# Kernel optimization log

Hardware: AMD Instinct MI355X
Metric: run time of the kernel (lower is better)

## Reference

```python
import jax, jax.numpy as jnp
import numpy as np
from jax import lax

B, T, C, H, W = 2, 64, 32, 64, 64   # (batch, feat-channels t, bands c, height, width)
NH = 4                              # num_heads; head dim = C//NH
HID = int(T * 2.66)                 # GDFN hidden channels = 170
EPS_LN = 1e-5
EPS_L2 = 1e-12


def _dwconv3d(x, w, pad):
    # x: (B, Cg, D, H, W); w: (Cg, 1, kd, kh, kw) depthwise
    cg = x.shape[1]
    return lax.conv_general_dilated(
        x, w, window_strides=(1, 1, 1), padding=pad,
        dimension_numbers=('NCDHW', 'OIDHW', 'NCDHW'),
        feature_group_count=cg)


def _pw(w, x):
    # 1x1x1 conv == channel GEMM; w: (out, in)
    return jnp.einsum('oi,bidhw->bodhw', w, x)


def _ln_ch(x, g, b):
    # LayerNorm over channel dim (dim1), matching reshape/transpose dance in torch
    m = jnp.mean(x, axis=1, keepdims=True)
    v = jnp.var(x, axis=1, keepdims=True)
    xn = (x - m) * lax.rsqrt(v + EPS_LN)
    return xn * g[None, :, None, None, None] + b[None, :, None, None, None]


def _attn(x, temperature, qkv_w, qkv_dw, attn_out_w):
    b, t, c, h, w = x.shape
    qkv = _dwconv3d(_pw(qkv_w, x), qkv_dw, ((0, 0), (1, 1), (1, 1)))  # (b,3t,c,h,w)
    q, k, v = jnp.split(qkv, 3, axis=1)
    L = h * w * t
    X = (t * c * h * w) // (NH * L)  # == c // NH
    rsh = lambda a: a.reshape(b, NH, X, L)
    q, k, v = rsh(q), rsh(k), rsh(v)
    l2n = lambda a: a / jnp.maximum(jnp.linalg.norm(a, axis=-1, keepdims=True), EPS_L2)
    q, k = l2n(q), l2n(k)
    scores = jnp.einsum('bnxl,bnyl->bnxy', q, k) * temperature  # (b,NH,X,X)
    att = jax.nn.softmax(scores, axis=-1)
    o = jnp.einsum('bnxy,bnyl->bnxl', att, v).reshape(b, t, c, h, w)
    return _pw(attn_out_w, o)


def _ffn(x, pin_w, dw_w, pout_w):
    y = _dwconv3d(_pw(pin_w, x), dw_w, ((1, 1), (1, 1), (1, 1)))  # (b,2*HID,c,h,w)
    x1, x2 = jnp.split(y, 2, axis=1)
    return _pw(pout_w, jax.nn.gelu(x1, approximate=False) * x2)


def setup_inputs() -> dict:
    key = jax.random.key(0)
    ks = jax.random.split(key, 12)
    s = lambda *sh: 1.0 / np.sqrt(np.prod(sh[1:]) if len(sh) > 1 else 1.0)
    p = lambda k, *sh: jax.random.normal(k, sh, dtype=jnp.float32) * s(*sh)
    return {
        'x': jax.random.normal(ks[0], (B, T, C, H, W), dtype=jnp.float32),
        'norm1_g': jnp.ones((T,), jnp.float32),
        'norm1_b': jnp.zeros((T,), jnp.float32),
        'temperature': jnp.ones((1, NH, 1, 1), jnp.float32),
        'qkv_w': p(ks[1], 3 * T, T),
        'qkv_dw': p(ks[2], 3 * T, 1, 1, 3, 3),
        'attn_out_w': p(ks[3], T, T),
        'norm2_g': jnp.ones((T,), jnp.float32),
        'norm2_b': jnp.zeros((T,), jnp.float32),
        'pin_w': p(ks[4], 2 * HID, T),
        'dw_w': p(ks[5], 2 * HID, 1, 3, 3, 3),
        'pout_w': p(ks[6], T, HID),
        'se_w': p(ks[7], T, T),
        'se_b': jnp.zeros((T,), jnp.float32),
    }


def reference(x, norm1_g, norm1_b, temperature, qkv_w, qkv_dw, attn_out_w,
              norm2_g, norm2_b, pin_w, dw_w, pout_w, se_w, se_b):
    x = x + _attn(_ln_ch(x, norm1_g, norm1_b), temperature, qkv_w, qkv_dw, attn_out_w)
    x = x + _ffn(_ln_ch(x, norm2_g, norm2_b), pin_w, dw_w, pout_w)
    s = jnp.mean(x, axis=(2, 3, 4), keepdims=True)               # GlobalAvgPool3d
    s = jax.nn.sigmoid(_pw(se_w, s) + se_b[None, :, None, None, None])
    return s * x
```

## Files before the change

kernel.cpp:

```cpp
#include <hip/hip_runtime.h>
#include <hip/hip_bf16.h>
#include <math.h>

typedef __hip_bfloat16 bf16;

#define S_ 131072

#define OFF_QKVW 0
#define OFF_AOW  12288
#define OFF_PINW 16384
#define OFF_POUTW 38912
#define OFF_SEW  49792
#define OFF_QDW  53888
#define OFF_DWW  55616
#define OFF_N1G  64796
#define OFF_N1B  64860
#define OFF_N2G  64924
#define OFF_N2B  64988
#define OFF_SEB  65052
#define OFF_TEMP 65116
#define WB_TOTAL 65120

#define SM_SSQ 0
#define SM_SSK 64
#define SM_ATT 128
#define SM_MEAN 640
#define SM_SVEC 768
#define SM_M 896
#define SM_FLAGI 9216

#define WSOFF_SM 262144
#define WSOFF_X1 303104
#define WSOFF_R  33857536
#define WS_REQUIRED 134520832ull

#define NCHUNK 256
#define PROW 44

__device__ __forceinline__ float toF(float v) { return v; }
__device__ __forceinline__ float toF(bf16 v) { return __bfloat162float(v); }

__device__ __forceinline__ float bfbitsToF(unsigned short u) {
  union { unsigned int i; float f; } x;
  x.i = ((unsigned int)u) << 16;
  return x.f;
}

__device__ __forceinline__ unsigned short bfBits(float f) {
  bf16 h = __float2bfloat16(f);
  return *reinterpret_cast<unsigned short*>(&h);
}

__device__ __forceinline__ float ldIn(const void* p, size_t i, int isbf) {
  return isbf ? __bfloat162float(((const bf16*)p)[i]) : ((const float*)p)[i];
}
__device__ __forceinline__ void stOut(void* p, size_t i, int isbf, float v) {
  if (isbf) ((bf16*)p)[i] = __float2bfloat16(v);
  else ((float*)p)[i] = v;
}

__device__ __forceinline__ float wred(float v) {
#pragma unroll
  for (int o = 32; o > 0; o >>= 1) v += __shfl_down(v, o, 64);
  return v;
}

__device__ __forceinline__ void conv4(const bf16* __restrict__ plane,
                                      const float* __restrict__ w9,
                                      int h, int w0, bool wlo, bool whi,
                                      float& o0, float& o1, float& o2, float& o3) {
  o0 = o1 = o2 = o3 = 0.f;
#pragma unroll
  for (int rr = 0; rr < 3; ++rr) {
    int hh = h - 1 + rr;
    if ((unsigned)hh < 64u) {
      const bf16* row = plane + hh * 64 + w0;
      ushort4 m = *reinterpret_cast<const ushort4*>(row);
      float v1 = bfbitsToF(m.x), v2 = bfbitsToF(m.y);
      float v3 = bfbitsToF(m.z), v4 = bfbitsToF(m.w);
      float v0 = wlo ? toF(row[-1]) : 0.f;
      float v5 = whi ? toF(row[4]) : 0.f;
      float wa = w9[rr * 3 + 0], wbb = w9[rr * 3 + 1], wc = w9[rr * 3 + 2];
      o0 = fmaf(wa, v0, fmaf(wbb, v1, fmaf(wc, v2, o0)));
      o1 = fmaf(wa, v1, fmaf(wbb, v2, fmaf(wc, v3, o1)));
      o2 = fmaf(wa, v2, fmaf(wbb, v3, fmaf(wc, v4, o2)));
      o3 = fmaf(wa, v3, fmaf(wbb, v4, fmaf(wc, v5, o3)));
    }
  }
}

__global__ void zero_sm(float* sm, const unsigned* n1g_raw) {
  for (int i = threadIdx.x; i < 768; i += 256) sm[i] = 0.f;
  if (threadIdx.x == 0) {
    ((int*)sm)[SM_FLAGI] = ((n1g_raw[0] & 0xFFFFu) != 0u) ? 1 : 0;
  }
}

__global__ void convert_w(const void* qkvw, const void* aow, const void* pinw,
                          const void* poutw, const void* sew, const void* qdw,
                          const void* dww, const void* n1g, const void* n1b,
                          const void* n2g, const void* n2b, const void* seb,
                          const void* temp, float* wb, const int* dflag) {
  int i = blockIdx.x * 256 + threadIdx.x;
  if (i >= WB_TOTAL) return;
  int f = *dflag;
  float v;
  if (i < OFF_AOW) v = ldIn(qkvw, i, f);
  else if (i < OFF_PINW) v = ldIn(aow, i - OFF_AOW, f);
  else if (i < OFF_POUTW) { int r = i - OFF_PINW; v = (r < 21760) ? ldIn(pinw, r, f) : 0.f; }
  else if (i < OFF_SEW) v = ldIn(poutw, i - OFF_POUTW, f);
  else if (i < OFF_QDW) v = ldIn(sew, i - OFF_SEW, f);
  else if (i < OFF_DWW) v = ldIn(qdw, i - OFF_QDW, f);
  else if (i < OFF_N1G) v = ldIn(dww, i - OFF_DWW, f);
  else if (i < OFF_N1B) v = ldIn(n1g, i - OFF_N1G, f);
  else if (i < OFF_N2G) v = ldIn(n1b, i - OFF_N1B, f);
  else if (i < OFF_N2B) v = ldIn(n2g, i - OFF_N2G, f);
  else if (i < OFF_SEB) v = ldIn(n2b, i - OFF_N2B, f);
  else if (i < OFF_TEMP) v = ldIn(seb, i - OFF_SEB, f);
  else v = ldIn(temp, i - OFF_TEMP, f);
  wb[i] = v;
}

__global__ __launch_bounds__(256) void qkv_ln_gemm(const void* __restrict__ x,
                                                   const float* __restrict__ wb,
                                                   bf16* __restrict__ qraw,
                                                   const int* __restrict__ dflag) {
  __shared__ bf16 tile[64][256];
  int tid = threadIdx.x;
  int p0 = blockIdx.x << 8;
  int b = p0 >> 17, s0 = p0 & (S_ - 1);
  int isbf = *dflag;
  float xin[64];
  if (isbf) {
    const bf16* src = (const bf16*)x + (size_t)b * 64 * S_ + s0;
#pragma unroll
    for (int i = 0; i < 8; ++i) {
      int q = i * 256 + tid;
      int row = q >> 5;
      int col8 = (q & 31) * 8;
      *reinterpret_cast<uint4*>(&tile[row][col8]) =
          *reinterpret_cast<const uint4*>(src + (size_t)row * S_ + col8);
    }
    __syncthreads();
#pragma unroll
    for (int t = 0; t < 64; ++t) xin[t] = toF(tile[t][tid]);
  } else {
    const float* xf = (const float*)x + (size_t)b * 64 * S_ + s0 + tid;
#pragma unroll
    for (int t = 0; t < 64; ++t) xin[t] = xf[(size_t)t * S_];
  }
  float sum = 0.f;
#pragma unroll
  for (int t = 0; t < 64; ++t) sum += xin[t];
  float mean = sum * (1.f / 64.f);
  float ss = 0.f;
#pragma unroll
  for (int t = 0; t < 64; ++t) { float d = xin[t] - mean; ss += d * d; }
  float rstd = rsqrtf(ss * (1.f / 64.f) + 1e-5f);
#pragma unroll
  for (int t = 0; t < 64; ++t)
    xin[t] = (xin[t] - mean) * rstd * wb[OFF_N1G + t] + wb[OFF_N1B + t];
  size_t obase = (size_t)b * 192 * S_ + s0 + tid;
  for (int oc = 0; oc < 192; oc += 16) {
    float acc[16];
#pragma unroll
    for (int j = 0; j < 16; ++j) acc[j] = 0.f;
    const float* wp = wb + OFF_QKVW + oc * 64;
#pragma unroll
    for (int t = 0; t < 64; ++t) {
      float xv = xin[t];
#pragma unroll
      for (int j = 0; j < 16; ++j) acc[j] = fmaf(wp[j * 64 + t], xv, acc[j]);
    }
#pragma unroll
    for (int j = 0; j < 16; ++j)
      qraw[obase + (size_t)(oc + j) * S_] = __float2bfloat16(acc[j]);
  }
}

__global__ __launch_bounds__(256, 4) void attn_scores(const bf16* __restrict__ qraw,
                                                      const float* __restrict__ wb,
                                                      float* __restrict__ part) {
  int blk = blockIdx.x;
  int bh = blk >> 9, qh = (blk >> 8) & 1, chunk = blk & (NCHUNK - 1);
  int b = bh >> 2, nh = bh & 3;
  int pbit = chunk >> 7;
  int c = (chunk >> 2) & 31;
  int hq = chunk & 3;
  int tid = threadIdx.x;
  int wseg = tid & 15, w0 = wseg * 4;
  int h = hq * 16 + (tid >> 4);
  bool wlo = (wseg != 0), whi = (wseg != 15);

  float dq[4], dk[8], dot[32], qv[4][4];
#pragma unroll
  for (int i = 0; i < 4; ++i) dq[i] = 0.f;
#pragma unroll
  for (int i = 0; i < 8; ++i) dk[i] = 0.f;
#pragma unroll
  for (int i = 0; i < 32; ++i) dot[i] = 0.f;

  const size_t bbase = ((size_t)(b * 192)) << 17;

#pragma unroll
  for (int r = 0; r < 4; ++r) {
    int ch = 2 * (nh * 8 + qh * 4 + r) + pbit;
    const bf16* pl = qraw + bbase + (((size_t)ch) << 17) + (c << 12);
    float o0, o1, o2, o3;
    conv4(pl, wb + OFF_QDW + ch * 9, h, w0, wlo, whi, o0, o1, o2, o3);
    qv[r][0] = o0; qv[r][1] = o1; qv[r][2] = o2; qv[r][3] = o3;
    dq[r] = fmaf(o0, o0, fmaf(o1, o1, fmaf(o2, o2, fmaf(o3, o3, dq[r]))));
  }
#pragma unroll
  for (int r = 0; r < 8; ++r) {
    int ch = 64 + 2 * (nh * 8 + r) + pbit;
    const bf16* pl = qraw + bbase + (((size_t)ch) << 17) + (c << 12);
    float k0, k1, k2, k3;
    conv4(pl, wb + OFF_QDW + ch * 9, h, w0, wlo, whi, k0, k1, k2, k3);
    dk[r] = fmaf(k0, k0, fmaf(k1, k1, fmaf(k2, k2, fmaf(k3, k3, dk[r]))));
#pragma unroll
    for (int i = 0; i < 4; ++i)
      dot[i * 8 + r] = fmaf(qv[i][0], k0, fmaf(qv[i][1], k1,
                       fmaf(qv[i][2], k2, fmaf(qv[i][3], k3, dot[i * 8 + r]))));
  }

  __shared__ float red[4][PROW];
  int lane = threadIdx.x & 63, wid = threadIdx.x >> 6;
#pragma unroll
  for (int i = 0; i < 4; ++i) {
    float v = wred(dq[i]);
    if (lane == 0) red[wid][i] = v;
  }
#pragma unroll
  for (int i = 0; i < 8; ++i) {
    float v = wred(dk[i]);
    if (lane == 0) red[wid][4 + i] = v;
  }
#pragma unroll
  for (int ij = 0; ij < 32; ++ij) {
    float v = wred(dot[ij]);
    if (lane == 0) red[wid][12 + ij] = v;
  }
  __syncthreads();
  if (threadIdx.x < PROW)
    part[blk * PROW + threadIdx.x] = red[0][threadIdx.x] + red[1][threadIdx.x] +
                                     red[2][threadIdx.x] + red[3][threadIdx.x];
}

__global__ void attn_reduce(const float* __restrict__ part, float* __restrict__ sm) {
  int o = blockIdx.x;
  int bh = o / 80, v = o - bh * 80;
  int qi, off;
  if (v < 8) {
    qi = v >> 2; off = v & 3;
  } else if (v < 16) {
    qi = 0; off = 4 + (v - 8);
  } else {
    int idx = v - 16;
    int i = idx >> 3, j = idx & 7;
    qi = i >> 2; off = 12 + (i & 3) * 8 + j;
  }
  __shared__ float s[256];
  s[threadIdx.x] = part[(((size_t)bh * 2 + qi) * NCHUNK + threadIdx.x) * PROW + off];
  __syncthreads();
#pragma unroll
  for (int st = 128; st > 0; st >>= 1) {
    if (threadIdx.x < st) s[threadIdx.x] += s[threadIdx.x + st];
    __syncthreads();
  }
  if (threadIdx.x == 0) {
    float r = s[0];
    if (v < 8) sm[SM_SSQ + bh * 8 + v] = r;
    else if (v < 16) sm[SM_SSK + bh * 8 + (v - 8)] = r;
    else sm[SM_ATT + bh * 64 + (v - 16)] = r;
  }
}

__global__ __launch_bounds__(256) void v_dwconv(const bf16* __restrict__ qraw,
                                                const float* __restrict__ wb,
                                                bf16* __restrict__ vc) {
  int blk = blockIdx.x;
  int hq = blk & 3, c = (blk >> 2) & 31, tv = (blk >> 7) & 63, b = blk >> 13;
  int tid = threadIdx.x;
  int wseg = tid & 15, w0 = wseg * 4;
  int h = hq * 16 + (tid >> 4);
  bool wlo = (wseg != 0), whi = (wseg != 15);
  const bf16* pl = qraw + (((size_t)(b * 192 + 128 + tv)) << 17) + (c << 12);
  float o0, o1, o2, o3;
  conv4(pl, wb + OFF_QDW + (128 + tv) * 9, h, w0, wlo, whi, o0, o1, o2, o3);
  bf16* dst = vc + (((size_t)(b * 64 + tv)) << 17) + (c << 12) + h * 64 + w0;
  ushort4 st;
  st.x = bfBits(o0); st.y = bfBits(o1); st.z = bfBits(o2); st.w = bfBits(o3);
  *reinterpret_cast<ushort4*>(dst) = st;
}

__global__ void attn_softmax_m(float* __restrict__ sm, const float* __restrict__ wb) {
  int t = threadIdx.x;
  if (t < 64) {
    int bh = t >> 3, i = t & 7, nh = bh & 3;
    float invq = 1.f / fmaxf(sqrtf(sm[SM_SSQ + bh * 8 + i]), 1e-12f);
    float temp = wb[OFF_TEMP + nh];
    float sc[8];
#pragma unroll
    for (int j = 0; j < 8; ++j) {
      float invk = 1.f / fmaxf(sqrtf(sm[SM_SSK + bh * 8 + j]), 1e-12f);
      sc[j] = sm[SM_ATT + bh * 64 + i * 8 + j] * invq * invk * temp;
    }
    float mx = sc[0];
#pragma unroll
    for (int j = 1; j < 8; ++j) mx = fmaxf(mx, sc[j]);
    float sum = 0.f;
#pragma unroll
    for (int j = 0; j < 8; ++j) { sc[j] = expf(sc[j] - mx); sum += sc[j]; }
    float inv = 1.f / sum;
#pragma unroll
    for (int j = 0; j < 8; ++j) sm[SM_ATT + bh * 64 + i * 8 + j] = sc[j] * inv;
  }
  __syncthreads();
  for (int k = 0; k < 32; ++k) {
    int idx = t + k * 256;
    int b = idx >> 12;
    int rest = idx & 4095;
    int tout = rest >> 6, tv = rest & 63;
    int n = (tv >> 4) & 3, j = (tv >> 1) & 7, pbit = tv & 1;
    float acc = 0.f;
#pragma unroll
    for (int i = 0; i < 8; ++i)
      acc = fmaf(wb[OFF_AOW + tout * 64 + ((n * 8 + i) * 2 + pbit)],
                 sm[SM_ATT + (b * 4 + n) * 64 + i * 8 + j], acc);
    sm[SM_M + b * 4096 + tv * 64 + tout] = acc;
  }
}

__global__ __launch_bounds__(256, 4) void attn_apply_gemm(const bf16* __restrict__ vc,
                                                          const float* __restrict__ sm,
                                                          const void* __restrict__ x,
                                                          bf16* __restrict__ x1,
                                                          const int* __restrict__ dflag) {
  int blk = blockIdx.x;
  int sblk = blk & 255, jh = (blk >> 8) & 1, b = blk >> 9;
  int s = (sblk << 9) | (threadIdx.x << 1);
  int isbf = *dflag;
  const bf16* ip = vc + (((size_t)(b * 64)) << 17) + s;
  const float* Mg = sm + SM_M + b * 4096 + jh * 32;
  float a0[32], a1[32];
#pragma unroll
  for (int j = 0; j < 32; ++j) { a0[j] = 0.f; a1[j] = 0.f; }

  float cx[4], cy[4];
#pragma unroll
  for (int u = 0; u < 4; ++u) {
    ushort2 m = *reinterpret_cast<const ushort2*>(ip + (size_t)u * S_);
    cx[u] = bfbitsToF(m.x); cy[u] = bfbitsToF(m.y);
  }
  for (int t = 0; t < 60; t += 4) {
    float nx[4], ny[4];
#pragma unroll
    for (int u = 0; u < 4; ++u) {
      ushort2 m = *reinterpret_cast<const ushort2*>(ip + (size_t)(t + 4 + u) * S_);
      nx[u] = bfbitsToF(m.x); ny[u] = bfbitsToF(m.y);
    }
#pragma unroll
    for (int u = 0; u < 4; ++u) {
      const float* mrow = Mg + (t + u) * 64;
#pragma unroll
      for (int j = 0; j < 32; ++j) {
        float wv = mrow[j];
        a0[j] = fmaf(wv, cx[u], a0[j]);
        a1[j] = fmaf(wv, cy[u], a1[j]);
      }
    }
#pragma unroll
    for (int u = 0; u < 4; ++u) { cx[u] = nx[u]; cy[u] = ny[u]; }
  }
#pragma unroll
  for (int u = 0; u < 4; ++u) {
    const float* mrow = Mg + (60 + u) * 64;
#pragma unroll
    for (int j = 0; j < 32; ++j) {
      float wv = mrow[j];
      a0[j] = fmaf(wv, cx[u], a0[j]);
      a1[j] = fmaf(wv, cy[u], a1[j]);
    }
  }

  size_t obase = (size_t)b * 64 * S_ + s;
#pragma unroll
  for (int j = 0; j < 32; ++j) {
    size_t oi = obase + (size_t)(jh * 32 + j) * S_;
    x1[oi]     = __float2bfloat16(a0[j] + ldIn(x, oi, isbf));
    x1[oi + 1] = __float2bfloat16(a1[j] + ldIn(x, oi + 1, isbf));
  }
}

__global__ __launch_bounds__(256) void pin_ln_gemm(const bf16* __restrict__ x1,
                                                   const float* __restrict__ wb,
                                                   bf16* __restrict__ slab, int c0) {
  __shared__ bf16 tile[64][256];
  int tid = threadIdx.x;
  int p0 = blockIdx.x << 8;
  int b = p0 >> 17, s0 = p0 & (S_ - 1);
  const bf16* src = x1 + (size_t)b * 64 * S_ + s0;
#pragma unroll
  for (int i = 0; i < 8; ++i) {
    int q = i * 256 + tid;
    int row = q >> 5;
    int col8 = (q & 31) * 8;
    *reinterpret_cast<uint4*>(&tile[row][col8]) =
        *reinterpret_cast<const uint4*>(src + (size_t)row * S_ + col8);
  }
  __syncthreads();

  float xin[64];
  float sum = 0.f;
#pragma unroll
  for (int t = 0; t < 64; ++t) { xin[t] = toF(tile[t][tid]); sum += xin[t]; }
  float mean = sum * (1.f / 64.f);
  float ss = 0.f;
#pragma unroll
  for (int t = 0; t < 64; ++t) { float d = xin[t] - mean; ss += d * d; }
  float rstd = rsqrtf(ss * (1.f / 64.f) + 1e-5f);
#pragma unroll
  for (int t = 0; t < 64; ++t)
    xin[t] = (xin[t] - mean) * rstd * wb[OFF_N2G + t] + wb[OFF_N2B + t];
  int s = s0 + tid;
  size_t obase = (size_t)b * 64 * S_ + s;
  for (int jc = 0; jc < 4; ++jc) {
    float acc[16];
    int rows[16];
#pragma unroll
    for (int jj = 0; jj < 16; ++jj) {
      acc[jj] = 0.f;
      int j = jc * 16 + jj;
      int c1 = c0 + (j & 31);
      rows[jj] = (c1 < 170) ? (c1 + ((j >= 32) ? 170 : 0)) : 0;
    }
#pragma unroll
    for (int t = 0; t < 64; ++t) {
      float xv = xin[t];
#pragma unroll
      for (int jj = 0; jj < 16; ++jj)
        acc[jj] = fmaf(wb[OFF_PINW + rows[jj] * 64 + t], xv, acc[jj]);
    }
#pragma unroll
    for (int jj = 0; jj < 16; ++jj) {
      int j = jc * 16 + jj;
      if (c0 + (j & 31) < 170)
        slab[obase + (size_t)j * S_] = __float2bfloat16(acc[jj]);
    }
  }
}

__global__ __launch_bounds__(256) void dw3d_gelu_chunk(const bf16* __restrict__ slab,
                                                       const float* __restrict__ wb,
                                                       bf16* __restrict__ g,
                                                       int c0, int nch) {
  int blk = blockIdx.x;
  int hq = blk & 3, c = (blk >> 2) & 31;
  int r = blk >> 7;
  int lj = r % nch, b = r / nch;
  int c1 = c0 + lj;
  int tid = threadIdx.x;
  int wseg = tid & 15, w0 = wseg * 4;
  int h = hq * 16 + (tid >> 4);
  bool wlo = (wseg != 0), whi = (wseg != 15);
  const bf16* p1 = slab + (((size_t)(b * 64 + lj)) << 17);
  const bf16* p2 = slab + (((size_t)(b * 64 + 32 + lj)) << 17);
  const float* w1 = wb + OFF_DWW + c1 * 27;
  const float* w2 = wb + OFF_DWW + (c1 + 170) * 27;
  float a10 = 0.f, a11 = 0.f, a12 = 0.f, a13 = 0.f;
  float a20 = 0.f, a21 = 0.f, a22 = 0.f, a23 = 0.f;
#pragma unroll
  for (int dc = -1; dc <= 1; ++dc) {
    int cc = c + dc;
    if ((unsigned)cc >= 32u) continue;
    const bf16* q1 = p1 + ((size_t)cc << 12);
    const bf16* q2 = p2 + ((size_t)cc << 12);
    const float* u1 = w1 + (dc + 1) * 9;
    const float* u2 = w2 + (dc + 1) * 9;
#pragma unroll
    for (int rr = 0; rr < 3; ++rr) {
      int hh = h - 1 + rr;
      if ((unsigned)hh < 64u) {
        const bf16* r1 = q1 + hh * 64 + w0;
        const bf16* r2 = q2 + hh * 64 + w0;
        ushort4 m1 = *reinterpret_cast<const ushort4*>(r1);
        ushort4 m2 = *reinterpret_cast<const ushort4*>(r2);
        float p0 = wlo ? toF(r1[-1]) : 0.f;
        float p5 = whi ? toF(r1[4]) : 0.f;
        float s0 = wlo ? toF(r2[-1]) : 0.f;
        float s5 = whi ? toF(r2[4]) : 0.f;
        float pa = bfbitsToF(m1.x), pb = bfbitsToF(m1.y);
        float pc = bfbitsToF(m1.z), pd = bfbitsToF(m1.w);
        float sa = bfbitsToF(m2.x), sb = bfbitsToF(m2.y);
        float sc = bfbitsToF(m2.z), sd = bfbitsToF(m2.w);
        float wa = u1[rr * 3 + 0], wbv = u1[rr * 3 + 1], wc = u1[rr * 3 + 2];
        a10 = fmaf(wa, p0, fmaf(wbv, pa, fmaf(wc, pb, a10)));
        a11 = fmaf(wa, pa, fmaf(wbv, pb, fmaf(wc, pc, a11)));
        a12 = fmaf(wa, pb, fmaf(wbv, pc, fmaf(wc, pd, a12)));
        a13 = fmaf(wa, pc, fmaf(wbv, pd, fmaf(wc, p5, a13)));
        float xa = u2[rr * 3 + 0], xb = u2[rr * 3 + 1], xc = u2[rr * 3 + 2];
        a20 = fmaf(xa, s0, fmaf(xb, sa, fmaf(xc, sb, a20)));
        a21 = fmaf(xa, sa, fmaf(xb, sb, fmaf(xc, sc, a21)));
        a22 = fmaf(xa, sb, fmaf(xb, sc, fmaf(xc, sd, a22)));
        a23 = fmaf(xa, sc, fmaf(xb, sd, fmaf(xc, s5, a23)));
      }
    }
  }
  float ge0 = 0.5f * a10 * (1.f + erff(a10 * 0.70710678118f));
  float ge1 = 0.5f * a11 * (1.f + erff(a11 * 0.70710678118f));
  float ge2 = 0.5f * a12 * (1.f + erff(a12 * 0.70710678118f));
  float ge3 = 0.5f * a13 * (1.f + erff(a13 * 0.70710678118f));
  int sp = (c << 12) + (h << 6) + w0;
  bf16* dst = g + (((size_t)(b * 170 + c1)) << 17) + sp;
  ushort4 st;
  st.x = bfBits(ge0 * a20); st.y = bfBits(ge1 * a21);
  st.z = bfBits(ge2 * a22); st.w = bfBits(ge3 * a23);
  *reinterpret_cast<ushort4*>(dst) = st;
}

__global__ __launch_bounds__(256, 2) void pout_gemm(const bf16* __restrict__ g,
                                                    const float* __restrict__ wb,
                                                    const bf16* __restrict__ x1,
                                                    void* __restrict__ out,
                                                    float* __restrict__ mean,
                                                    const int* __restrict__ dflag) {
  int blk = blockIdx.x;
  int sblk = blk & 127, jh = (blk >> 7) & 1, b = blk >> 8;
  int s = (sblk << 10) | (threadIdx.x << 2);
  int isbf = *dflag;
  const bf16* ip = g + (size_t)b * 170 * S_ + s;
  const float* wp = wb + OFF_POUTW + (jh * 32) * 170;
  float a0[32], a1[32], a2[32], a3[32];
#pragma unroll
  for (int j = 0; j < 32; ++j) { a0[j] = 0.f; a1[j] = 0.f; a2[j] = 0.f; a3[j] = 0.f; }

  float c0[4], c1[4], c2[4], c3[4];
#pragma unroll
  for (int u = 0; u < 4; ++u) {
    ushort4 m = *reinterpret_cast<const ushort4*>(ip + (size_t)u * S_);
    c0[u] = bfbitsToF(m.x); c1[u] = bfbitsToF(m.y);
    c2[u] = bfbitsToF(m.z); c3[u] = bfbitsToF(m.w);
  }
  for (int t = 0; t < 168; t += 4) {
    float n0[4], n1[4], n2[4], n3[4];
#pragma unroll
    for (int u = 0; u < 4; ++u) {
      ushort4 m = *reinterpret_cast<const ushort4*>(ip + (size_t)(t + 4 + u) * S_);
      n0[u] = bfbitsToF(m.x); n1[u] = bfbitsToF(m.y);
      n2[u] = bfbitsToF(m.z); n3[u] = bfbitsToF(m.w);
    }
#pragma unroll
    for (int u = 0; u < 4; ++u) {
#pragma unroll
      for (int j = 0; j < 32; ++j) {
        float wv = wp[j * 170 + t + u];
        a0[j] = fmaf(wv, c0[u], a0[j]);
        a1[j] = fmaf(wv, c1[u], a1[j]);
        a2[j] = fmaf(wv, c2[u], a2[j]);
        a3[j] = fmaf(wv, c3[u], a3[j]);
      }
    }
#pragma unroll
    for (int u = 0; u < 4; ++u) { c0[u] = n0[u]; c1[u] = n1[u]; c2[u] = n2[u]; c3[u] = n3[u]; }
  }
#pragma unroll
  for (int u = 0; u < 2; ++u) {
#pragma unroll
    for (int j = 0; j < 32; ++j) {
      float wv = wp[j * 170 + 168 + u];
      a0[j] = fmaf(wv, c0[u], a0[j]);
      a1[j] = fmaf(wv, c1[u], a1[j]);
      a2[j] = fmaf(wv, c2[u], a2[j]);
      a3[j] = fmaf(wv, c3[u], a3[j]);
    }
  }

  __shared__ float red[4][32];
  int lane = threadIdx.x & 63, wid = threadIdx.x >> 6;
  size_t obase = (size_t)b * 64 * S_ + s;
#pragma unroll
  for (int j = 0; j < 32; ++j) {
    size_t oi = obase + (size_t)(jh * 32 + j) * S_;
    ushort4 rm = *reinterpret_cast<const ushort4*>(x1 + oi);
    float v0 = a0[j] + bfbitsToF(rm.x);
    float v1 = a1[j] + bfbitsToF(rm.y);
    float v2 = a2[j] + bfbitsToF(rm.z);
    float v3 = a3[j] + bfbitsToF(rm.w);
    stOut(out, oi,     isbf, v0);
    stOut(out, oi + 1, isbf, v1);
    stOut(out, oi + 2, isbf, v2);
    stOut(out, oi + 3, isbf, v3);
    float v = wred(v0 + v1 + v2 + v3);
    if (lane == 0) red[wid][j] = v;
  }
  __syncthreads();
  if (threadIdx.x < 32) {
    float tot = red[0][threadIdx.x] + red[1][threadIdx.x] +
                red[2][threadIdx.x] + red[3][threadIdx.x];
    atomicAdd(&mean[b * 64 + jh * 32 + threadIdx.x], tot * (1.f / S_));
  }
}

__global__ void se_vec(const float* __restrict__ wb, float* __restrict__ sm) {
  int t = threadIdx.x;
  int b = t >> 6, o = t & 63;
  float acc = wb[OFF_SEB + o];
  for (int k = 0; k < 64; ++k)
    acc = fmaf(wb[OFF_SEW + o * 64 + k], sm[SM_MEAN + b * 64 + k], acc);
  sm[SM_SVEC + t] = 1.f / (1.f + expf(-acc));
}

__global__ __launch_bounds__(256) void se_scale(void* __restrict__ xo,
                                                const float* __restrict__ svec,
                                                const int* __restrict__ dflag) {
  size_t i4 = ((size_t)blockIdx.x * 256 + threadIdx.x) * 4;
  int row = (int)(i4 >> 17);
  int isbf = *dflag;
  float sv = svec[row];
  if (isbf) {
    bf16* p = (bf16*)xo + i4;
    ushort4 m = *reinterpret_cast<ushort4*>(p);
    m.x = bfBits(bfbitsToF(m.x) * sv);
    m.y = bfBits(bfbitsToF(m.y) * sv);
    m.z = bfBits(bfbitsToF(m.z) * sv);
    m.w = bfBits(bfbitsToF(m.w) * sv);
    *reinterpret_cast<ushort4*>(p) = m;
  } else {
    float4* p = reinterpret_cast<float4*>((float*)xo + i4);
    float4 m = *p;
    m.x *= sv; m.y *= sv; m.z *= sv; m.w *= sv;
    *p = m;
  }
}

extern "C" void kernel_launch(void* const* d_in, const int* in_sizes, int n_in,
                              void* d_out, int out_size, void* d_ws, size_t ws_size,
                              hipStream_t stream) {
  if (ws_size < WS_REQUIRED) return;

  char* ws = (char*)d_ws;
  float* WB  = (float*)ws;
  float* SM  = (float*)(ws + WSOFF_SM);
  const int* FLAG = (const int*)(SM + SM_FLAGI);
  bf16*  X1  = (bf16*)(ws + WSOFF_X1);
  float* PART= (float*)(ws + WSOFF_X1);
  bf16*  QR  = (bf16*)(ws + WSOFF_R);
  bf16*  G   = (bf16*)(ws + WSOFF_R);
  bf16*  SLAB= (bf16*)d_out;
  bf16*  VC  = (bf16*)d_out;

  zero_sm<<<1, 256, 0, stream>>>(SM, (const unsigned*)d_in[1]);
  convert_w<<<(WB_TOTAL + 255) / 256, 256, 0, stream>>>(
      d_in[4], d_in[6], d_in[9], d_in[11], d_in[12], d_in[5], d_in[10],
      d_in[1], d_in[2], d_in[7], d_in[8], d_in[13], d_in[3], WB, FLAG);

  qkv_ln_gemm<<<1024, 256, 0, stream>>>(d_in[0], WB, QR, FLAG);
  attn_scores<<<8 * 2 * NCHUNK, 256, 0, stream>>>(QR, WB, PART);
  attn_reduce<<<640, 256, 0, stream>>>(PART, SM);
  v_dwconv<<<16384, 256, 0, stream>>>(QR, WB, VC);
  attn_softmax_m<<<1, 256, 0, stream>>>(SM, WB);
  attn_apply_gemm<<<1024, 256, 0, stream>>>(VC, SM, d_in[0], X1, FLAG);

  for (int c0 = 0; c0 < 170; c0 += 32) {
    int nch = (170 - c0 < 32) ? (170 - c0) : 32;
    pin_ln_gemm<<<1024, 256, 0, stream>>>(X1, WB, SLAB, c0);
    dw3d_gelu_chunk<<<nch * 256, 256, 0, stream>>>(SLAB, WB, G, c0, nch);
  }
  pout_gemm<<<512, 256, 0, stream>>>(G, WB, X1, d_out, SM + SM_MEAN, FLAG);

  se_vec<<<1, 128, 0, stream>>>(WB, SM);
  se_scale<<<16384, 256, 0, stream>>>(d_out, SM + SM_SVEC, FLAG);
}
```

Before: 1.339 ms.

## Restructure attention-apply GEMM to stage input tile in LDS with 64 outputs per thread

```diff
diff --git a/kernel.cpp b/kernel.cpp
--- a/kernel.cpp
+++ b/kernel.cpp
@@ -332,64 +332,43 @@
   }
 }
 
-__global__ __launch_bounds__(256, 4) void attn_apply_gemm(const bf16* __restrict__ vc,
-                                                          const float* __restrict__ sm,
-                                                          const void* __restrict__ x,
-                                                          bf16* __restrict__ x1,
-                                                          const int* __restrict__ dflag) {
-  int blk = blockIdx.x;
-  int sblk = blk & 255, jh = (blk >> 8) & 1, b = blk >> 9;
-  int s = (sblk << 9) | (threadIdx.x << 1);
+__global__ __launch_bounds__(256) void attn_apply_gemm(const bf16* __restrict__ vc,
+                                                       const float* __restrict__ sm,
+                                                       const void* __restrict__ x,
+                                                       bf16* __restrict__ x1,
+                                                       const int* __restrict__ dflag) {
+  __shared__ bf16 tile[64][256];
+  int tid = threadIdx.x;
+  int p0 = blockIdx.x << 8;
+  int b = p0 >> 17, s0 = p0 & (S_ - 1);
   int isbf = *dflag;
-  const bf16* ip = vc + (((size_t)(b * 64)) << 17) + s;
-  const float* Mg = sm + SM_M + b * 4096 + jh * 32;
-  float a0[32], a1[32];
-#pragma unroll
-  for (int j = 0; j < 32; ++j) { a0[j] = 0.f; a1[j] = 0.f; }
-
-  float cx[4], cy[4];
-#pragma unroll
-  for (int u = 0; u < 4; ++u) {
-    ushort2 m = *reinterpret_cast<const ushort2*>(ip + (size_t)u * S_);
-    cx[u] = bfbitsToF(m.x); cy[u] = bfbitsToF(m.y);
-  }
-  for (int t = 0; t < 60; t += 4) {
-    float nx[4], ny[4];
-#pragma unroll
-    for (int u = 0; u < 4; ++u) {
-      ushort2 m = *reinterpret_cast<const ushort2*>(ip + (size_t)(t + 4 + u) * S_);
-      nx[u] = bfbitsToF(m.x); ny[u] = bfbitsToF(m.y);
-    }
-#pragma unroll
-    for (int u = 0; u < 4; ++u) {
-      const float* mrow = Mg + (t + u) * 64;
-#pragma unroll
-      for (int j = 0; j < 32; ++j) {
-        float wv = mrow[j];
-        a0[j] = fmaf(wv, cx[u], a0[j]);
-        a1[j] = fmaf(wv, cy[u], a1[j]);
-      }
-    }
-#pragma unroll
-    for (int u = 0; u < 4; ++u) { cx[u] = nx[u]; cy[u] = ny[u]; }
-  }
-#pragma unroll
-  for (int u = 0; u < 4; ++u) {
-    const float* mrow = Mg + (60 + u) * 64;
-#pragma unroll
-    for (int j = 0; j < 32; ++j) {
-      float wv = mrow[j];
-      a0[j] = fmaf(wv, cx[u], a0[j]);
-      a1[j] = fmaf(wv, cy[u], a1[j]);
-    }
-  }
-
-  size_t obase = (size_t)b * 64 * S_ + s;
-#pragma unroll
-  for (int j = 0; j < 32; ++j) {
-    size_t oi = obase + (size_t)(jh * 32 + j) * S_;
-    x1[oi]     = __float2bfloat16(a0[j] + ldIn(x, oi, isbf));
-    x1[oi + 1] = __float2bfloat16(a1[j] + ldIn(x, oi + 1, isbf));
+  const bf16* src = vc + (((size_t)(b * 64)) << 17) + s0;
+#pragma unroll
+  for (int i = 0; i < 8; ++i) {
+    int q = i * 256 + tid;
+    int row = q >> 5;
+    int col8 = (q & 31) * 8;
+    *reinterpret_cast<uint4*>(&tile[row][col8]) =
+        *reinterpret_cast<const uint4*>(src + (size_t)row * S_ + col8);
+  }
+  __syncthreads();
+
+  const float* Mg = sm + SM_M + b * 4096;
+  float acc[64];
+#pragma unroll
+  for (int j = 0; j < 64; ++j) acc[j] = 0.f;
+  for (int t = 0; t < 64; ++t) {
+    float v = toF(tile[t][tid]);
+    const float* mrow = Mg + t * 64;
+#pragma unroll
+    for (int j = 0; j < 64; ++j) acc[j] = fmaf(mrow[j], v, acc[j]);
+  }
+
+  size_t obase = (size_t)b * 64 * S_ + s0 + tid;
+#pragma unroll
+  for (int j = 0; j < 64; ++j) {
+    size_t oi = obase + (size_t)j * S_;
+    x1[oi] = __float2bfloat16(acc[j] + ldIn(x, oi, isbf));
   }
 }
 
```

After: 1.341 ms. Within noise of the previous version (+0.2%).
